# Performance work log

Hardware: AMD Instinct MI355X
Metric: run time of the kernel (lower is better)

## Reference

```python
import jax, jax.numpy as jnp
import numpy as np

N = 100000
E = 1600000
IN_C, HID_C, OUT_C = 128, 128, 64


def setup_inputs() -> dict:
    key = jax.random.key(0)
    ks = jax.random.split(key, 8)
    x = jax.random.normal(ks[0], (N, IN_C), dtype=jnp.float32)
    edge_index = jax.random.randint(ks[1], (2, E), 0, N, dtype=jnp.int64)
    # Glorot-ish init for the 3 GCNConv linear weights + zero biases (PyG default)
    def glorot(k, fan_in, fan_out):
        s = jnp.sqrt(6.0 / (fan_in + fan_out))
        return jax.random.uniform(k, (fan_in, fan_out), jnp.float32, -s, s)
    return {
        "x": x,
        "edge_index": edge_index,
        "W1": glorot(ks[2], IN_C, HID_C), "b1": jnp.zeros((HID_C,), jnp.float32),
        "W2": glorot(ks[3], HID_C, HID_C), "b2": jnp.zeros((HID_C,), jnp.float32),
        "W3": glorot(ks[4], HID_C, OUT_C), "b3": jnp.zeros((OUT_C,), jnp.float32),
    }


def _gcn_norm(edge_index, num_nodes):
    # add self loops, compute D^-1/2 (A+I) D^-1/2 edge coefficients (PyG gcn_norm)
    loop = jnp.arange(num_nodes, dtype=edge_index.dtype)
    src = jnp.concatenate([edge_index[0], loop])  # [E+N]
    dst = jnp.concatenate([edge_index[1], loop])
    w = jnp.ones_like(src, dtype=jnp.float32)
    deg = jax.ops.segment_sum(w, dst, num_segments=num_nodes)
    dinv = jnp.where(deg > 0, jax.lax.rsqrt(deg), 0.0)
    norm = dinv[src] * dinv[dst]  # [E+N]
    return src, dst, norm


def _gcn_layer(x, src, dst, norm, W, b, num_nodes):
    h = x @ W                                   # [N, out]
    msg = h[src] * norm[:, None]                # gather + scale, [E+N, out]
    agg = jax.ops.segment_sum(msg, dst, num_segments=num_nodes)  # scatter-add
    return agg + b


def reference(x, edge_index, W1, b1, W2, b2, W3, b3):
    src, dst, norm = _gcn_norm(edge_index, N)
    h = jax.nn.relu(_gcn_layer(x, src, dst, norm, W1, b1, N))
    h = jax.nn.relu(_gcn_layer(h, src, dst, norm, W2, b2, N))
    h = _gcn_layer(h, src, dst, norm, W3, b3, N)
    return jax.nn.log_softmax(h, axis=-1)  # [N, OUT_C]
```

## Files before the change

kernel.cpp:

```cpp
#include <hip/hip_runtime.h>
#include <hip/hip_bf16.h>


constexpr int N_NODES = 100000;
constexpr int E_EDGES = 1600000;
constexpr int NB = (N_NODES + 127) / 128;
constexpr int BCAP = 2560;
constexpr int CHUNK = 4096;
constexpr int NCHUNK = (E_EDGES + CHUNK - 1) / CHUNK;
constexpr int NGRP = N_NODES / 8;

typedef short bf16x8 __attribute__((ext_vector_type(8)));
typedef float f32x4 __attribute__((ext_vector_type(4)));

__device__ __forceinline__ unsigned short f2bf(float f) {
    unsigned u = __float_as_uint(f);
    unsigned r = (u + 0x7fff + ((u >> 16) & 1)) >> 16;
    return (unsigned short)r;
}
__device__ __forceinline__ float bf_lo(unsigned u) { return __uint_as_float(u << 16); }
__device__ __forceinline__ float bf_hi(unsigned u) { return __uint_as_float(u & 0xffff0000u); }
__device__ __forceinline__ unsigned pack2bf(float lo, float hi) {
    return (unsigned)f2bf(lo) | ((unsigned)f2bf(hi) << 16);
}

__device__ __forceinline__ int get_idx(const void* ei, int use64, long long pos) {
    if (use64) return (int)((const long long*)ei)[pos];
    return ((const int*)ei)[pos];
}

__global__ void prep_wt_kernel(const float* __restrict__ W1, const float* __restrict__ W2,
                               const float* __restrict__ W3,
                               unsigned short* __restrict__ WT1,
                               unsigned short* __restrict__ WT2,
                               unsigned short* __restrict__ WT3,
                               const int* __restrict__ ei32, int* __restrict__ flag,
                               int* __restrict__ cursorPad) {
    const int b = blockIdx.x;
    if (b == 3) {
        for (int i = threadIdx.x; i < NB * 16; i += blockDim.x) cursorPad[i] = 0;
        if (threadIdx.x == 0) {
            int ok64 = 1;
#pragma unroll
            for (int i = 1; i < 64; i += 2) ok64 &= (ei32[i] == 0);
            *flag = ok64;
        }
        return;
    }
    const float* W = (b == 0) ? W1 : (b == 1) ? W2 : W3;
    unsigned short* WT = (b == 0) ? WT1 : (b == 1) ? WT2 : WT3;
    const int COUT = (b == 2) ? 64 : 128;
    for (int i = threadIdx.x; i < COUT * 128; i += blockDim.x) {
        int c = i >> 7;
        int k = i & 127;
        WT[c * 128 + k] = f2bf(W[k * COUT + c]);
    }
}

__global__ __launch_bounds__(256) void scatter_direct(
    const void* __restrict__ ei, const int* __restrict__ flag,
    int* __restrict__ cursorPad, unsigned* __restrict__ pairs) {
    __shared__ int h[NB];
    __shared__ int base[NB];
    __shared__ unsigned dstb[CHUNK];
    const int t = threadIdx.x;
    const int use64 = *flag;
    const int e0 = blockIdx.x * CHUNK;
    const int e1 = min(E_EDGES, e0 + CHUNK);

    for (int i = t; i < NB; i += 256) h[i] = 0;
    __syncthreads();
    for (int e = e0 + t; e < e1; e += 256) {
        unsigned d = (unsigned)get_idx(ei, use64, (long long)E_EDGES + e);
        dstb[e - e0] = d;
        atomicAdd(&h[d >> 7], 1);
    }
    __syncthreads();
    for (int i = t; i < NB; i += 256) {
        int c = h[i];
        if (c) base[i] = atomicAdd(&cursorPad[i * 16], c);
        h[i] = 0;
    }
    __syncthreads();
    for (int e = e0 + t; e < e1; e += 256) {
        unsigned s = (unsigned)get_idx(ei, use64, e);
        unsigned d = dstb[e - e0];
        int b = d >> 7;
        int r = base[b] + atomicAdd(&h[b], 1);
        if (r < BCAP) pairs[(unsigned)b * BCAP + r] = (s << 7) | (d & 127u);
    }
}

__global__ __launch_bounds__(256) void fine_sort_kernel(
    const unsigned* __restrict__ pairs, const int* __restrict__ cursorPad,
    int* __restrict__ csr, int* __restrict__ rowptr, int* __restrict__ deg,
    float* __restrict__ dinv) {
    __shared__ int h[128];
    __shared__ int rp[128];
    __shared__ int sc[128];
    const int t = threadIdx.x;
    const int b = blockIdx.x;
    const int base = b * BCAP;
    const int cnt = min(cursorPad[b * 16], BCAP);

    if (t < 128) h[t] = 0;
    __syncthreads();
    for (int i = t; i < cnt; i += 256) {
        unsigned p = pairs[base + i];
        atomicAdd(&h[p & 127u], 1);
    }
    __syncthreads();
    int v = (t < 128) ? h[t] : 0;
    if (t < 128) sc[t] = v;
    __syncthreads();
    int incl = v;
    for (int off = 1; off < 128; off <<= 1) {
        int add = (t >= off && t < 128) ? sc[t - off] : 0;
        __syncthreads();
        if (t < 128) {
            incl += add;
            sc[t] = incl;
        }
        __syncthreads();
    }
    if (t < 128) {
        rp[t] = incl - v;
        int node = b * 128 + t;
        if (node < N_NODES) {
            rowptr[node] = base + incl - v;
            deg[node] = v;
            dinv[node] = rsqrtf((float)(v + 1));
        }
        h[t] = 0;
    }
    __syncthreads();
    for (int i = t; i < cnt; i += 256) {
        unsigned p = pairs[base + i];
        int l = (int)(p & 127u);
        int r = atomicAdd(&h[l], 1);
        csr[base + rp[l] + r] = (int)(p >> 7);
    }
}

template <int COUT>
__global__ __launch_bounds__(256) void gemm_mfma_f32(const float* __restrict__ X,
                                                     const unsigned short* __restrict__ WT,
                                                     const float* __restrict__ dinv,
                                                     unsigned short* __restrict__ H) {
    constexpr int NT = COUT / 16;
    __shared__ short Albs[64 * 128];
    __shared__ short Wlds[COUT * 128];

    const int t = threadIdx.x;
    const int row0 = blockIdx.x * 64;

    for (int i = t; i < COUT * 16; i += 256) {
        int n = i >> 4, k8 = i & 15;
        bf16x8 v = *(const bf16x8*)&WT[n * 128 + k8 * 8];
        int ns = (n & ~15) | ((n & 15) ^ k8);
        *(bf16x8*)&Wlds[(k8 * COUT + ns) * 8] = v;
    }
    for (int i = t; i < 1024; i += 256) {
        int m = i >> 4, k8 = i & 15;
        int gr = min(row0 + m, N_NODES - 1);
        const float* p = &X[(size_t)gr * 128 + k8 * 8];
        float4 f0 = *(const float4*)p;
        float4 f1 = *(const float4*)(p + 4);
        bf16x8 v;
        v[0] = (short)f2bf(f0.x); v[1] = (short)f2bf(f0.y);
        v[2] = (short)f2bf(f0.z); v[3] = (short)f2bf(f0.w);
        v[4] = (short)f2bf(f1.x); v[5] = (short)f2bf(f1.y);
        v[6] = (short)f2bf(f1.z); v[7] = (short)f2bf(f1.w);
        int u = ((m >> 4) * 16 + k8) * 16 + ((m & 15) ^ k8);
        *(bf16x8*)&Albs[u * 8] = v;
    }
    __syncthreads();

    const int lane = t & 63;
    const int wv = t >> 6;
    const int l15 = lane & 15;
    const int quad = lane >> 4;

    f32x4 acc[NT];
#pragma unroll
    for (int ct = 0; ct < NT; ct++) acc[ct] = (f32x4){0.f, 0.f, 0.f, 0.f};

#pragma unroll
    for (int kcg = 0; kcg < 4; kcg++) {
        const int k8 = kcg * 4 + quad;
        bf16x8 a = *(const bf16x8*)&Albs[((wv * 16 + k8) * 16 + (l15 ^ k8)) * 8];
#pragma unroll
        for (int ct = 0; ct < NT; ct++) {
            bf16x8 b = *(const bf16x8*)&Wlds[(k8 * COUT + ct * 16 + (l15 ^ k8)) * 8];
            acc[ct] = __builtin_amdgcn_mfma_f32_16x16x32_bf16(a, b, acc[ct], 0, 0, 0);
        }
    }

    const int m0 = row0 + wv * 16;
#pragma unroll
    for (int r = 0; r < 4; r++) {
        int m = m0 + quad * 4 + r;
        if (m < N_NODES) {
            float dv = dinv[m];
#pragma unroll
            for (int ct = 0; ct < NT; ct++)
                H[(size_t)m * COUT + ct * 16 + l15] = f2bf(acc[ct][r] * dv);
        } else if (m == N_NODES) {
#pragma unroll
            for (int ct = 0; ct < NT; ct++)
                H[(size_t)m * COUT + ct * 16 + l15] = 0;
        }
    }
}

template <int COUT>
__global__ __launch_bounds__(256) void agg128_fused_p(
    const unsigned short* __restrict__ Hb, const int* __restrict__ rowptr,
    const int* __restrict__ deg, const int* __restrict__ csr,
    const float* __restrict__ dinv, const float* __restrict__ bias,
    const unsigned short* __restrict__ WT, unsigned short* __restrict__ Hn) {
    constexpr int NT = COUT / 16;
    constexpr int CTW = NT / 4;
    __shared__ short Wlds[COUT * 128];
    __shared__ short Atile[16 * 128];

    const int t = threadIdx.x;

    for (int i = t; i < COUT * 16; i += 256) {
        int nn = i >> 4, k8 = i & 15;
        bf16x8 v = *(const bf16x8*)&WT[nn * 128 + k8 * 8];
        int ns = (nn & ~15) | ((nn & 15) ^ k8);
        *(bf16x8*)&Wlds[(k8 * COUT + ns) * 8] = v;
    }
    if (t < 128) {
        int k8z = t >> 3, mm = 8 + (t & 7);
        *(uint4*)&Atile[(k8z * 16 + (mm ^ k8z)) * 8] = (uint4){0u, 0u, 0u, 0u};
    }
    if (blockIdx.x == 0 && t < COUT / 4)
        *(unsigned long long*)((char*)Hn + (size_t)N_NODES * (COUT * 2) + t * 8) = 0ull;

    const int lane = t & 63;
    const int wv = t >> 6;
    const int li = lane & 31;
    const int half = lane >> 5;
    const unsigned li8 = (unsigned)li * 8u;
    const char* Hc = (const char*)Hb;
    const int l15 = lane & 15;
    const int quad = lane >> 4;

    __syncthreads();

    for (int g = blockIdx.x; g < NGRP; g += gridDim.x) {
        const int n = g * 8 + wv * 2 + half;

        uint2 s = *(const uint2*)(Hc + (size_t)n * 256u + li8);
        float a0 = bf_lo(s.x), a1 = bf_hi(s.x), a2 = bf_lo(s.y), a3 = bf_hi(s.y);

        const int start = rowptr[n];
        const int dc = deg[n];
        const int dmax = max(dc, __shfl_xor(dc, 32));

        for (int eb = 0; eb < dmax; eb += 32) {
            int myidx = N_NODES;
            if (eb + li < dc) myidx = csr[start + eb + li];
            const int jmax = min(32, dmax - eb);
            int j = 0;
            for (; j + 16 <= jmax; j += 16) {
                int idx[16];
                uint2 u[16];
#pragma unroll
                for (int q = 0; q < 16; q++) idx[q] = __shfl(myidx, j + q, 32);
#pragma unroll
                for (int q = 0; q < 16; q++)
                    u[q] = *(const uint2*)(Hc + (((unsigned)idx[q] << 8) + li8));
#pragma unroll
                for (int q = 0; q < 16; q++) {
                    a0 += bf_lo(u[q].x); a1 += bf_hi(u[q].x);
                    a2 += bf_lo(u[q].y); a3 += bf_hi(u[q].y);
                }
            }
            for (; j + 8 <= jmax; j += 8) {
                int idx[8];
                uint2 u[8];
#pragma unroll
                for (int q = 0; q < 8; q++) idx[q] = __shfl(myidx, j + q, 32);
#pragma unroll
                for (int q = 0; q < 8; q++)
                    u[q] = *(const uint2*)(Hc + (((unsigned)idx[q] << 8) + li8));
#pragma unroll
                for (int q = 0; q < 8; q++) {
                    a0 += bf_lo(u[q].x); a1 += bf_hi(u[q].x);
                    a2 += bf_lo(u[q].y); a3 += bf_hi(u[q].y);
                }
            }
            for (; j + 4 <= jmax; j += 4) {
                int idx[4];
                uint2 u[4];
#pragma unroll
                for (int q = 0; q < 4; q++) idx[q] = __shfl(myidx, j + q, 32);
#pragma unroll
                for (int q = 0; q < 4; q++)
                    u[q] = *(const uint2*)(Hc + (((unsigned)idx[q] << 8) + li8));
#pragma unroll
                for (int q = 0; q < 4; q++) {
                    a0 += bf_lo(u[q].x); a1 += bf_hi(u[q].x);
                    a2 += bf_lo(u[q].y); a3 += bf_hi(u[q].y);
                }
            }
            for (; j < jmax; j++) {
                int i0 = __shfl(myidx, j, 32);
                uint2 u0 = *(const uint2*)(Hc + (((unsigned)i0 << 8) + li8));
                a0 += bf_lo(u0.x); a1 += bf_hi(u0.x);
                a2 += bf_lo(u0.y); a3 += bf_hi(u0.y);
            }
        }

        {
            const float dn = dinv[n];
            float4 bv = *(const float4*)((const char*)bias + li * 16);
            unsigned w0 = pack2bf(fmaxf(a0 * dn + bv.x, 0.f), fmaxf(a1 * dn + bv.y, 0.f));
            unsigned w1 = pack2bf(fmaxf(a2 * dn + bv.z, 0.f), fmaxf(a3 * dn + bv.w, 0.f));
            const int r = wv * 2 + half;
            const int k8 = li >> 1;
            uint2 o; o.x = w0; o.y = w1;
            *(uint2*)&Atile[(k8 * 16 + (r ^ k8)) * 8 + (li & 1) * 4] = o;
        }
        __syncthreads();

        f32x4 acc[CTW];
#pragma unroll
        for (int c = 0; c < CTW; c++) acc[c] = (f32x4){0.f, 0.f, 0.f, 0.f};

#pragma unroll
        for (int kcg = 0; kcg < 4; kcg++) {
            const int k8 = kcg * 4 + quad;
            bf16x8 a = *(const bf16x8*)&Atile[(k8 * 16 + (l15 ^ k8)) * 8];
#pragma unroll
            for (int c = 0; c < CTW; c++) {
                const int ct = wv * CTW + c;
                bf16x8 b = *(const bf16x8*)&Wlds[(k8 * COUT + ct * 16 + (l15 ^ k8)) * 8];
                acc[c] = __builtin_amdgcn_mfma_f32_16x16x32_bf16(a, b, acc[c], 0, 0, 0);
            }
        }

#pragma unroll
        for (int rr = 0; rr < 4; rr++) {
            const int row = quad * 4 + rr;
            if (row < 8) {
                const int m = g * 8 + row;
                const float dv = dinv[m];
#pragma unroll
                for (int c = 0; c < CTW; c++) {
                    const int ct = wv * CTW + c;
                    Hn[(size_t)m * COUT + ct * 16 + l15] = f2bf(acc[c][rr] * dv);
                }
            }
        }
        __syncthreads();
    }
}

__global__ __launch_bounds__(256) void aggregate64_lsm_pair(
    const unsigned short* __restrict__ Hb, const int* __restrict__ rowptr,
    const int* __restrict__ deg, const int* __restrict__ csr,
    const float* __restrict__ dinv, const float* __restrict__ bias,
    float* __restrict__ out) {
    const int lane = threadIdx.x & 63;
    const int wv = threadIdx.x >> 6;
    const int li = lane & 31;
    const int half = lane >> 5;
    const int n = blockIdx.x * 8 + wv * 2 + half;
    const unsigned li4 = (unsigned)li * 4u;
    const char* Hc = (const char*)Hb;

    unsigned s = *(const unsigned*)(Hc + (size_t)n * 128u + li4);
    float a0 = bf_lo(s), a1 = bf_hi(s);

    const int start = rowptr[n];
    const int dc = deg[n];
    const int dmax = max(dc, __shfl_xor(dc, 32));

    for (int eb = 0; eb < dmax; eb += 32) {
        int myidx = N_NODES;
        if (eb + li < dc) myidx = csr[start + eb + li];
        const int jmax = min(32, dmax - eb);
        int j = 0;
        for (; j + 16 <= jmax; j += 16) {
            int idx[16];
            unsigned u[16];
#pragma unroll
            for (int q = 0; q < 16; q++) idx[q] = __shfl(myidx, j + q, 32);
#pragma unroll
            for (int q = 0; q < 16; q++)
                u[q] = *(const unsigned*)(Hc + (((unsigned)idx[q] << 7) + li4));
#pragma unroll
            for (int q = 0; q < 16; q++) { a0 += bf_lo(u[q]); a1 += bf_hi(u[q]); }
        }
        for (; j + 8 <= jmax; j += 8) {
            int idx[8];
            unsigned u[8];
#pragma unroll
            for (int q = 0; q < 8; q++) idx[q] = __shfl(myidx, j + q, 32);
#pragma unroll
            for (int q = 0; q < 8; q++)
                u[q] = *(const unsigned*)(Hc + (((unsigned)idx[q] << 7) + li4));
#pragma unroll
            for (int q = 0; q < 8; q++) { a0 += bf_lo(u[q]); a1 += bf_hi(u[q]); }
        }
        for (; j + 4 <= jmax; j += 4) {
            int idx[4];
            unsigned u[4];
#pragma unroll
            for (int q = 0; q < 4; q++) idx[q] = __shfl(myidx, j + q, 32);
#pragma unroll
            for (int q = 0; q < 4; q++)
                u[q] = *(const unsigned*)(Hc + (((unsigned)idx[q] << 7) + li4));
#pragma unroll
            for (int q = 0; q < 4; q++) { a0 += bf_lo(u[q]); a1 += bf_hi(u[q]); }
        }
        for (; j < jmax; j++) {
            int i0 = __shfl(myidx, j, 32);
            unsigned u0 = *(const unsigned*)(Hc + (((unsigned)i0 << 7) + li4));
            a0 += bf_lo(u0); a1 += bf_hi(u0);
        }
    }

    const float dn = dinv[n];
    float2 bv = *(const float2*)((const char*)bias + li * 8);
    float v0 = a0 * dn + bv.x;
    float v1 = a1 * dn + bv.y;

    float m = fmaxf(v0, v1);
#pragma unroll
    for (int off = 16; off; off >>= 1) m = fmaxf(m, __shfl_xor(m, off));
    float e = expf(v0 - m) + expf(v1 - m);
#pragma unroll
    for (int off = 16; off; off >>= 1) e += __shfl_xor(e, off);
    float lse = m + logf(e);
    float2 o = make_float2(v0 - lse, v1 - lse);
    *(float2*)((char*)out + (size_t)n * 256 + li * 8) = o;
}

extern "C" void kernel_launch(void* const* d_in, const int* in_sizes, int n_in,
                              void* d_out, int out_size, void* d_ws, size_t ws_size,
                              hipStream_t stream) {
    const float* x = (const float*)d_in[0];
    const void* ei = d_in[1];
    const float* W1 = (const float*)d_in[2];
    const float* b1 = (const float*)d_in[3];
    const float* W2 = (const float*)d_in[4];
    const float* b2 = (const float*)d_in[5];
    const float* W3 = (const float*)d_in[6];
    const float* b3 = (const float*)d_in[7];
    float* out = (float*)d_out;

    char* w = (char*)d_ws;
    size_t off = 0;
    auto take = [&](size_t bytes) {
        char* p = w + off;
        off = (off + bytes + 255) & ~(size_t)255;
        return p;
    };
    int* flag = (int*)take(4);
    int* cursorPad = (int*)take((size_t)NB * 64);
    int* deg = (int*)take((size_t)N_NODES * 4);
    int* rowptr = (int*)take((size_t)N_NODES * 4);
    float* dinv = (float*)take((size_t)N_NODES * 4);
    int* csr = (int*)take((size_t)NB * BCAP * 4);
    unsigned short* WT1 = (unsigned short*)take(128 * 128 * 2);
    unsigned short* WT2 = (unsigned short*)take(128 * 128 * 2);
    unsigned short* WT3 = (unsigned short*)take(64 * 128 * 2);
    unsigned short* A = (unsigned short*)take((size_t)(N_NODES + 1) * 128 * 2);
    unsigned short* B = (unsigned short*)take((size_t)(N_NODES + 1) * 128 * 2);
    unsigned* pairs = (unsigned*)A;

    prep_wt_kernel<<<4, 256, 0, stream>>>(W1, W2, W3, WT1, WT2, WT3,
                                          (const int*)ei, flag, cursorPad);
    scatter_direct<<<NCHUNK, 256, 0, stream>>>(ei, flag, cursorPad, pairs);
    fine_sort_kernel<<<NB, 256, 0, stream>>>(pairs, cursorPad, csr, rowptr, deg, dinv);

    const int gg = (N_NODES + 63) / 64;
    const int g8 = N_NODES / 8;

    gemm_mfma_f32<128><<<gg, 256, 0, stream>>>(x, WT1, dinv, A);
    agg128_fused_p<128><<<1024, 256, 0, stream>>>(A, rowptr, deg, csr, dinv, b1, WT2, B);
    agg128_fused_p<64><<<2048, 256, 0, stream>>>(B, rowptr, deg, csr, dinv, b2, WT3, A);
    aggregate64_lsm_pair<<<g8, 256, 0, stream>>>(A, rowptr, deg, csr, dinv, b3, out);
}
```

Before: 367.5 us.

## Process nodes in degree-sorted order to balance per-wave aggregation work

Builds a degree histogram during the CSR fine sort, prefix-sums it, and scatters node ids into a degree-sorted permutation. All aggregation kernels then map groups of nodes through this permutation, so the paired half-waves and wave groups handle nodes of similar degree. This is meant to cut divergence, where a half-wave idles while its partner processes a longer edge list. The cost is two extra small kernel launches, global atomics on the histogram, an extra indirection per node, and less locality in the output writes.

New measurement: 908.5 us. +147.2%, slower.

```diff
diff --git a/kernel.cpp b/kernel.cpp
--- a/kernel.cpp
+++ b/kernel.cpp
@@ -35,10 +35,11 @@
                                unsigned short* __restrict__ WT2,
                                unsigned short* __restrict__ WT3,
                                const int* __restrict__ ei32, int* __restrict__ flag,
-                               int* __restrict__ cursorPad) {
+                               int* __restrict__ cursorPad, int* __restrict__ hist) {
     const int b = blockIdx.x;
     if (b == 3) {
         for (int i = threadIdx.x; i < NB * 16; i += blockDim.x) cursorPad[i] = 0;
+        if (threadIdx.x < 256) hist[threadIdx.x] = 0;
         if (threadIdx.x == 0) {
             int ok64 = 1;
 #pragma unroll
@@ -94,7 +95,7 @@
 __global__ __launch_bounds__(256) void fine_sort_kernel(
     const unsigned* __restrict__ pairs, const int* __restrict__ cursorPad,
     int* __restrict__ csr, int* __restrict__ rowptr, int* __restrict__ deg,
-    float* __restrict__ dinv) {
+    float* __restrict__ dinv, int* __restrict__ hist) {
     __shared__ int h[128];
     __shared__ int rp[128];
     __shared__ int sc[128];
@@ -130,6 +131,7 @@
             rowptr[node] = base + incl - v;
             deg[node] = v;
             dinv[node] = rsqrtf((float)(v + 1));
+            atomicAdd(&hist[min(v, 255)], 1);
         }
         h[t] = 0;
     }
@@ -139,6 +141,34 @@
         int l = (int)(p & 127u);
         int r = atomicAdd(&h[l], 1);
         csr[base + rp[l] + r] = (int)(p >> 7);
+    }
+}
+
+__global__ __launch_bounds__(256) void hist_prefix_kernel(const int* __restrict__ hist,
+                                                          int* __restrict__ cursor) {
+    __shared__ int sc[256];
+    const int t = threadIdx.x;
+    int v = hist[t];
+    sc[t] = v;
+    __syncthreads();
+    int incl = v;
+    for (int off = 1; off < 256; off <<= 1) {
+        int add = (t >= off) ? sc[t - off] : 0;
+        __syncthreads();
+        incl += add;
+        sc[t] = incl;
+        __syncthreads();
+    }
+    cursor[t] = incl - v;
+}
+
+__global__ __launch_bounds__(256) void perm_scatter_kernel(const int* __restrict__ deg,
+                                                           int* __restrict__ cursor,
+                                                           int* __restrict__ perm) {
+    const int n = blockIdx.x * 256 + threadIdx.x;
+    if (n < N_NODES) {
+        int pos = atomicAdd(&cursor[min(deg[n], 255)], 1);
+        perm[pos] = n;
     }
 }
 
@@ -218,7 +248,8 @@
     const unsigned short* __restrict__ Hb, const int* __restrict__ rowptr,
     const int* __restrict__ deg, const int* __restrict__ csr,
     const float* __restrict__ dinv, const float* __restrict__ bias,
-    const unsigned short* __restrict__ WT, unsigned short* __restrict__ Hn) {
+    const unsigned short* __restrict__ WT, const int* __restrict__ perm,
+    unsigned short* __restrict__ Hn) {
     constexpr int NT = COUT / 16;
     constexpr int CTW = NT / 4;
     __shared__ short Wlds[COUT * 128];
@@ -251,7 +282,7 @@
     __syncthreads();
 
     for (int g = blockIdx.x; g < NGRP; g += gridDim.x) {
-        const int n = g * 8 + wv * 2 + half;
+        const int n = perm[g * 8 + wv * 2 + half];
 
         uint2 s = *(const uint2*)(Hc + (size_t)n * 256u + li8);
         float a0 = bf_lo(s.x), a1 = bf_hi(s.x), a2 = bf_lo(s.y), a3 = bf_hi(s.y);
@@ -347,7 +378,7 @@
         for (int rr = 0; rr < 4; rr++) {
             const int row = quad * 4 + rr;
             if (row < 8) {
-                const int m = g * 8 + row;
+                const int m = perm[g * 8 + row];
                 const float dv = dinv[m];
 #pragma unroll
                 for (int c = 0; c < CTW; c++) {
@@ -364,12 +395,12 @@
     const unsigned short* __restrict__ Hb, const int* __restrict__ rowptr,
     const int* __restrict__ deg, const int* __restrict__ csr,
     const float* __restrict__ dinv, const float* __restrict__ bias,
-    float* __restrict__ out) {
+    const int* __restrict__ perm, float* __restrict__ out) {
     const int lane = threadIdx.x & 63;
     const int wv = threadIdx.x >> 6;
     const int li = lane & 31;
     const int half = lane >> 5;
-    const int n = blockIdx.x * 8 + wv * 2 + half;
+    const int n = perm[blockIdx.x * 8 + wv * 2 + half];
     const unsigned li4 = (unsigned)li * 4u;
     const char* Hc = (const char*)Hb;
 
@@ -463,6 +494,9 @@
     };
     int* flag = (int*)take(4);
     int* cursorPad = (int*)take((size_t)NB * 64);
+    int* hist = (int*)take(256 * 4);
+    int* cursor = (int*)take(256 * 4);
+    int* perm = (int*)take((size_t)N_NODES * 4);
     int* deg = (int*)take((size_t)N_NODES * 4);
     int* rowptr = (int*)take((size_t)N_NODES * 4);
     float* dinv = (float*)take((size_t)N_NODES * 4);
@@ -475,15 +509,17 @@
     unsigned* pairs = (unsigned*)A;
 
     prep_wt_kernel<<<4, 256, 0, stream>>>(W1, W2, W3, WT1, WT2, WT3,
-                                          (const int*)ei, flag, cursorPad);
+                                          (const int*)ei, flag, cursorPad, hist);
     scatter_direct<<<NCHUNK, 256, 0, stream>>>(ei, flag, cursorPad, pairs);
-    fine_sort_kernel<<<NB, 256, 0, stream>>>(pairs, cursorPad, csr, rowptr, deg, dinv);
+    fine_sort_kernel<<<NB, 256, 0, stream>>>(pairs, cursorPad, csr, rowptr, deg, dinv, hist);
+    hist_prefix_kernel<<<1, 256, 0, stream>>>(hist, cursor);
+    perm_scatter_kernel<<<(N_NODES + 255) / 256, 256, 0, stream>>>(deg, cursor, perm);
 
     const int gg = (N_NODES + 63) / 64;
     const int g8 = N_NODES / 8;
 
     gemm_mfma_f32<128><<<gg, 256, 0, stream>>>(x, WT1, dinv, A);
-    agg128_fused_p<128><<<1024, 256, 0, stream>>>(A, rowptr, deg, csr, dinv, b1, WT2, B);
-    agg128_fused_p<64><<<2048, 256, 0, stream>>>(B, rowptr, deg, csr, dinv, b2, WT3, A);
-    aggregate64_lsm_pair<<<g8, 256, 0, stream>>>(A, rowptr, deg, csr, dinv, b3, out);
-}
+    agg128_fused_p<128><<<1024, 256, 0, stream>>>(A, rowptr, deg, csr, dinv, b1, WT2, perm, B);
+    agg128_fused_p<64><<<2048, 256, 0, stream>>>(B, rowptr, deg, csr, dinv, b2, WT3, perm, A);
+    aggregate64_lsm_pair<<<g8, 256, 0, stream>>>(A, rowptr, deg, csr, dinv, b3, perm, out);
+}
```
